# Kernel optimization log

Hardware: AMD Instinct MI355X
Metric: run time of the kernel (lower is better)

The kernel has to match this reference:

```python
import jax, jax.numpy as jnp
import numpy as np

N = 8192        # batch_size == num nodes == num hyperedges
D = 512         # hidden_dim
H_HEADS = 8
HD = D // H_HEADS
TOP_K = 16
EPS = 1e-5      # LayerNorm eps


def setup_inputs() -> dict:
    key = jax.random.key(0)
    ks = jax.random.split(key, 10)
    def rn(k, shape, scale=0.02):
        return jax.random.normal(k, shape, dtype=jnp.float32) * scale
    return {
        "x0": jax.random.normal(ks[0], (N, D), dtype=jnp.float32),
        "x1": jax.random.normal(ks[1], (N, D), dtype=jnp.float32),
        # modality projections: Linear -> ReLU -> LayerNorm (per modality)
        "w_p0": rn(ks[2], (D, D)), "b_p0": jnp.zeros((D,), jnp.float32),
        "g0": jnp.ones((D,), jnp.float32), "beta0": jnp.zeros((D,), jnp.float32),
        "w_p1": rn(ks[3], (D, D)), "b_p1": jnp.zeros((D,), jnp.float32),
        "g1": jnp.ones((D,), jnp.float32), "beta1": jnp.zeros((D,), jnp.float32),
        # MultiheadAttention packed in-proj + out-proj
        "in_w": rn(ks[4], (3 * D, D)), "in_b": jnp.zeros((3 * D,), jnp.float32),
        "out_w": rn(ks[5], (D, D)), "out_b": jnp.zeros((D,), jnp.float32),
        # edge weight predictor MLP
        "ew_w1": rn(ks[6], (D // 2, D)), "ew_b1": jnp.zeros((D // 2,), jnp.float32),
        "ew_w2": rn(ks[7], (1, D // 2)), "ew_b2": jnp.zeros((1,), jnp.float32),
    }


def _layernorm(x, g, b):
    m = x.mean(-1, keepdims=True)
    v = ((x - m) ** 2).mean(-1, keepdims=True)
    return (x - m) * jax.lax.rsqrt(v + EPS) * g + b


def _forward(x0, x1, w_p0, b_p0, g0, beta0, w_p1, b_p1, g1, beta1,
             in_w, in_b, out_w, out_b, ew_w1, ew_b1, ew_w2, ew_b2):
    # per-modality projection: Linear -> ReLU -> LayerNorm
    p0 = _layernorm(jax.nn.relu(x0 @ w_p0.T + b_p0), g0, beta0)
    p1 = _layernorm(jax.nn.relu(x1 @ w_p1.T + b_p1), g1, beta1)
    seq = jnp.stack([p0, p1], axis=1)                       # [N, 2, D]
    # cross-modal MHA (self-attention over the 2 modality tokens)
    qkv = seq @ in_w.T + in_b                               # [N, 2, 3D]
    q, k, v = jnp.split(qkv, 3, axis=-1)
    q = q.reshape(N, 2, H_HEADS, HD)
    k = k.reshape(N, 2, H_HEADS, HD)
    v = v.reshape(N, 2, H_HEADS, HD)
    scores = jnp.einsum('bqhd,bkhd->bhqk', q, k) / jnp.sqrt(jnp.float32(HD))
    attn = jax.nn.softmax(scores, axis=-1)                  # [N, h, 2, 2]
    ctx = jnp.einsum('bhqk,bkhd->bqhd', attn, v).reshape(N, 2, D)
    attended = ctx @ out_w.T + out_b                        # [N, 2, D]
    fused = attended.mean(axis=1)                           # [N, D]
    # node-node attention similarity, row-softmax
    sim = jax.nn.softmax(fused @ fused.T, axis=1)           # [N, N]
    _, idx = jax.lax.top_k(sim, TOP_K)                      # [N, K]
    vals = jnp.take_along_axis(sim, idx, axis=1)            # [N, K]
    rows = jnp.arange(N)
    # H[i,i]=1 first, then H[neighbor, i] = sim[i, neighbor] (may overwrite diag)
    H = jnp.zeros((N, N), sim.dtype).at[rows, rows].set(1.0)
    H = H.at[idx, rows[:, None]].set(vals)
    colsum = H.sum(axis=0)
    H = H.at[rows, rows].set(jnp.where(colsum == 0, 1.0, H[rows, rows]))
    # edge weights
    hidden = jax.nn.relu(fused @ ew_w1.T + ew_b1)
    ew = jax.nn.sigmoid(hidden @ ew_w2.T + ew_b2)[:, 0]     # [N]
    ew = jnp.maximum(ew, 1e-8)
    return H, ew


def reference(x0, x1, w_p0, b_p0, g0, beta0, w_p1, b_p1, g1, beta1,
              in_w, in_b, out_w, out_b, ew_w1, ew_b1, ew_w2, ew_b2):
    return _forward(x0, x1, w_p0, b_p0, g0, beta0, w_p1, b_p1, g1, beta1,
                    in_w, in_b, out_w, out_b, ew_w1, ew_b1, ew_w2, ew_b2)
```

## Files before the change

### kernel.cpp

```cpp
#include <hip/hip_runtime.h>
#include <hip/hip_bf16.h>

#define NN 8192
#define DD 512

typedef unsigned short u16;
typedef __bf16 bf16_t;
typedef bf16_t bf16x8 __attribute__((ext_vector_type(8)));
typedef float f32x4 __attribute__((ext_vector_type(4)));

__device__ __forceinline__ float bf2f(u16 h) {
    union { unsigned u; float f; } v; v.u = ((unsigned)h) << 16; return v.f;
}
__device__ __forceinline__ float bflo(unsigned u) {
    union { unsigned u; float f; } v; v.u = u << 16; return v.f;
}
__device__ __forceinline__ float bfhi(unsigned u) {
    union { unsigned u; float f; } v; v.u = u & 0xFFFF0000u; return v.f;
}
__device__ __forceinline__ u16 f2bf(float f) {
    union { float f; unsigned u; } v; v.f = f;
    unsigned r = v.u + 0x7fffu + ((v.u >> 16) & 1u);
    return (u16)(r >> 16);
}

__global__ __launch_bounds__(256) void cvt7(
        const float* __restrict__ s0, u16* __restrict__ d0,
        const float* __restrict__ s1, u16* __restrict__ d1,
        const float* __restrict__ s2, u16* __restrict__ d2,
        const float* __restrict__ s3, u16* __restrict__ d3,
        const float* __restrict__ s4, u16* __restrict__ d4,
        const float* __restrict__ s5, u16* __restrict__ d5,
        const float* __restrict__ s6, u16* __restrict__ d6) {
    size_t v = ((size_t)blockIdx.x * 256 + threadIdx.x) * 8;
    const float* s; u16* d; size_t off;
    if (v < 4194304)      { s = s0; d = d0; off = v; }
    else if (v < 8388608) { s = s1; d = d1; off = v - 4194304; }
    else if (v < 8650752) { s = s2; d = d2; off = v - 8388608; }
    else if (v < 8912896) { s = s3; d = d3; off = v - 8650752; }
    else if (v < 9699328) { s = s4; d = d4; off = v - 8912896; }
    else if (v < 9961472) { s = s5; d = d5; off = v - 9699328; }
    else                  { s = s6; d = d6; off = v - 9961472; }
    float4 a = *(const float4*)(s + off);
    float4 b = *(const float4*)(s + off + 4);
    ushort4 o0 = make_ushort4(f2bf(a.x), f2bf(a.y), f2bf(a.z), f2bf(a.w));
    ushort4 o1 = make_ushort4(f2bf(b.x), f2bf(b.y), f2bf(b.z), f2bf(b.w));
    *(ushort4*)(d + off) = o0;
    *(ushort4*)(d + off + 4) = o1;
}

#define EPS_LDS 136
template<bool RELU, bool BIAS, bool SPLIT>
__global__ __launch_bounds__(256) void gemm_bt(const u16* __restrict__ A,
        const u16* __restrict__ B, const float* __restrict__ bias,
        const u16* __restrict__ B2, const float* __restrict__ bias2, int halfY,
        u16* __restrict__ C, int M, int Nc, int K) {
    __shared__ alignas(16) u16 Smem[128 * EPS_LDS];
    u16* As = Smem;
    u16* Bs = Smem + 128 * 64;
    const int t = threadIdx.x;
    const int lane = t & 63;
    const int wave = t >> 6;
    const int wm = (wave >> 1) * 64;
    const int wn = (wave & 1) * 64;
    const int rowA = blockIdx.y * 128;
    const int rowB = blockIdx.x * 128;
    if (SPLIT && (int)blockIdx.y >= halfY) { B = B2; bias = bias2; }

    f32x4 acc[4][4] = {};
    const int mrow = lane & 15;
    const int kk = (lane >> 4) * 8;

    for (int k0 = 0; k0 < K; k0 += 64) {
        __syncthreads();
        #pragma unroll
        for (int r = 0; r < 4; ++r) {
            int chunk = r * 256 + t;
            const u16* srcA = A + (size_t)(rowA + (chunk >> 3)) * K + k0 + (chunk & 7) * 8;
            __builtin_amdgcn_global_load_lds(
                (const __attribute__((address_space(1))) void*)srcA,
                (__attribute__((address_space(3))) void*)(As + chunk * 8), 16, 0, 0);
            const u16* srcB = B + (size_t)(rowB + (chunk >> 3)) * K + k0 + (chunk & 7) * 8;
            __builtin_amdgcn_global_load_lds(
                (const __attribute__((address_space(1))) void*)srcB,
                (__attribute__((address_space(3))) void*)(Bs + chunk * 8), 16, 0, 0);
        }
        __syncthreads();
        #pragma unroll
        for (int ks = 0; ks < 64; ks += 32) {
            bf16x8 af[4], bfv[4];
            #pragma unroll
            for (int i = 0; i < 4; ++i)
                af[i] = *(const bf16x8*)(As + (wm + i * 16 + mrow) * 64 + ks + kk);
            #pragma unroll
            for (int j = 0; j < 4; ++j)
                bfv[j] = *(const bf16x8*)(Bs + (wn + j * 16 + mrow) * 64 + ks + kk);
            #pragma unroll
            for (int i = 0; i < 4; ++i)
                #pragma unroll
                for (int j = 0; j < 4; ++j)
                    acc[i][j] = __builtin_amdgcn_mfma_f32_16x16x32_bf16(af[i], bfv[j], acc[i][j], 0, 0, 0);
        }
    }

    __syncthreads();
    const int er0 = wm + (lane >> 4) * 4;
    const int ec0 = wn + (lane & 15);
    #pragma unroll
    for (int j = 0; j < 4; ++j) {
        int c = ec0 + j * 16;
        float bv = BIAS ? bias[rowB + c] : 0.0f;
        #pragma unroll
        for (int i = 0; i < 4; ++i) {
            #pragma unroll
            for (int r = 0; r < 4; ++r) {
                float v = acc[i][j][r] + bv;
                if (RELU) v = fmaxf(v, 0.0f);
                Smem[(er0 + i * 16 + r) * EPS_LDS + c] = f2bf(v);
            }
        }
    }
    __syncthreads();
    #pragma unroll
    for (int pass = 0; pass < 8; ++pass) {
        int chunk = pass * 256 + t;
        int rloc = chunk >> 4, coff = (chunk & 15) * 8;
        bf16x8 v = *(const bf16x8*)(Smem + rloc * EPS_LDS + coff);
        *(bf16x8*)(C + (size_t)(rowA + rloc) * Nc + rowB + coff) = v;
    }
}

#define SYM_LDS 129
__global__ __launch_bounds__(256) void gemm_sym(const u16* __restrict__ F,
        u16* __restrict__ C) {
    __shared__ alignas(16) u16 Smem[128 * SYM_LDS];
    const int bx = blockIdx.x, by = blockIdx.y;
    if (bx < by) return;
    u16* As = Smem;
    u16* Bs = Smem + 128 * 64;
    const int t = threadIdx.x;
    const int lane = t & 63;
    const int wave = t >> 6;
    const int wm = (wave >> 1) * 64;
    const int wn = (wave & 1) * 64;
    const int rowI = by * 128;
    const int rowJ = bx * 128;

    f32x4 acc[4][4] = {};
    const int mrow = lane & 15;
    const int kk = (lane >> 4) * 8;

    for (int k0 = 0; k0 < DD; k0 += 64) {
        __syncthreads();
        #pragma unroll
        for (int r = 0; r < 4; ++r) {
            int chunk = r * 256 + t;
            const u16* srcA = F + (size_t)(rowI + (chunk >> 3)) * DD + k0 + (chunk & 7) * 8;
            __builtin_amdgcn_global_load_lds(
                (const __attribute__((address_space(1))) void*)srcA,
                (__attribute__((address_space(3))) void*)(As + chunk * 8), 16, 0, 0);
            const u16* srcB = F + (size_t)(rowJ + (chunk >> 3)) * DD + k0 + (chunk & 7) * 8;
            __builtin_amdgcn_global_load_lds(
                (const __attribute__((address_space(1))) void*)srcB,
                (__attribute__((address_space(3))) void*)(Bs + chunk * 8), 16, 0, 0);
        }
        __syncthreads();
        #pragma unroll
        for (int ks = 0; ks < 64; ks += 32) {
            bf16x8 af[4], bfv[4];
            #pragma unroll
            for (int i = 0; i < 4; ++i)
                af[i] = *(const bf16x8*)(As + (wm + i * 16 + mrow) * 64 + ks + kk);
            #pragma unroll
            for (int j = 0; j < 4; ++j)
                bfv[j] = *(const bf16x8*)(Bs + (wn + j * 16 + mrow) * 64 + ks + kk);
            #pragma unroll
            for (int i = 0; i < 4; ++i)
                #pragma unroll
                for (int j = 0; j < 4; ++j)
                    acc[i][j] = __builtin_amdgcn_mfma_f32_16x16x32_bf16(af[i], bfv[j], acc[i][j], 0, 0, 0);
        }
    }

    __syncthreads();
    const int er0 = wm + (lane >> 4) * 4;
    const int ec0 = wn + (lane & 15);
    #pragma unroll
    for (int j = 0; j < 4; ++j) {
        int c = ec0 + j * 16;
        #pragma unroll
        for (int i = 0; i < 4; ++i) {
            #pragma unroll
            for (int r = 0; r < 4; ++r)
                Smem[(er0 + i * 16 + r) * SYM_LDS + c] = f2bf(acc[i][j][r]);
        }
    }
    __syncthreads();
    #pragma unroll
    for (int pass = 0; pass < 8; ++pass) {
        int chunk = pass * 256 + t;
        int rloc = chunk >> 4, coff = (chunk & 15) * 8;
        union { u16 us[8]; bf16x8 v; } buf;
        #pragma unroll
        for (int k = 0; k < 8; ++k) buf.us[k] = Smem[rloc * SYM_LDS + coff + k];
        *(bf16x8*)(C + (size_t)(rowI + rloc) * NN + rowJ + coff) = buf.v;
    }
    if (bx != by) {
        #pragma unroll
        for (int pass = 0; pass < 8; ++pass) {
            int chunk = pass * 256 + t;
            int tr = chunk >> 4, roff = (chunk & 15) * 8;
            union { u16 us[8]; bf16x8 v; } buf;
            #pragma unroll
            for (int k = 0; k < 8; ++k) buf.us[k] = Smem[(roff + k) * SYM_LDS + tr];
            *(bf16x8*)(C + (size_t)(rowJ + tr) * NN + rowI + roff) = buf.v;
        }
    }
}

__global__ __launch_bounds__(256) void ln2_kernel(const u16* __restrict__ y,
        const float* __restrict__ g0, const float* __restrict__ b0,
        const float* __restrict__ g1, const float* __restrict__ b1,
        u16* __restrict__ seq) {
    __shared__ float sred[4];
    int n = blockIdx.x, t = threadIdx.x;
    int modality = n >> 13, node = n & (NN - 1);
    const float* g = modality ? g1 : g0;
    const float* b = modality ? b1 : b0;
    const u16* yr = y + (size_t)n * DD;
    float x0 = bf2f(yr[t]), x1 = bf2f(yr[t + 256]);
    float s = x0 + x1;
    for (int off = 32; off; off >>= 1) s += __shfl_xor(s, off);
    if ((t & 63) == 0) sred[t >> 6] = s;
    __syncthreads();
    float mean = (sred[0] + sred[1] + sred[2] + sred[3]) * (1.0f / DD);
    __syncthreads();
    float d0 = x0 - mean, d1 = x1 - mean;
    float vs = d0 * d0 + d1 * d1;
    for (int off = 32; off; off >>= 1) vs += __shfl_xor(vs, off);
    if ((t & 63) == 0) sred[t >> 6] = vs;
    __syncthreads();
    float var = (sred[0] + sred[1] + sred[2] + sred[3]) * (1.0f / DD);
    float inv = rsqrtf(var + 1e-5f);
    u16* out = seq + (size_t)node * (2 * DD) + modality * DD;
    out[t]       = f2bf(d0 * inv * g[t]       + b[t]);
    out[t + 256] = f2bf(d1 * inv * g[t + 256] + b[t + 256]);
}

__global__ __launch_bounds__(256) void attn_kernel(const u16* __restrict__ qkv,
        u16* __restrict__ ctxm) {
    int gid = blockIdx.x * 4 + (threadIdx.x >> 6);
    int lane = threadIdx.x & 63;
    int n = gid >> 3, h = gid & 7;
    const u16* r0 = qkv + (size_t)(n * 2) * 1536;
    const u16* r1 = r0 + 1536;
    float q0 = bf2f(r0[h * 64 + lane]);
    float k0 = bf2f(r0[512 + h * 64 + lane]);
    float v0 = bf2f(r0[1024 + h * 64 + lane]);
    float q1 = bf2f(r1[h * 64 + lane]);
    float k1 = bf2f(r1[512 + h * 64 + lane]);
    float v1 = bf2f(r1[1024 + h * 64 + lane]);
    float p00 = q0 * k0, p01 = q0 * k1, p10 = q1 * k0, p11 = q1 * k1;
    for (int off = 32; off; off >>= 1) {
        p00 += __shfl_xor(p00, off);
        p01 += __shfl_xor(p01, off);
        p10 += __shfl_xor(p10, off);
        p11 += __shfl_xor(p11, off);
    }
    const float sc = 0.125f;
    float s00 = p00 * sc, s01 = p01 * sc, s10 = p10 * sc, s11 = p11 * sc;
    float m0 = fmaxf(s00, s01), e00 = __expf(s00 - m0), e01 = __expf(s01 - m0);
    float a00 = e00 / (e00 + e01), a01 = e01 / (e00 + e01);
    float m1 = fmaxf(s10, s11), e10 = __expf(s10 - m1), e11 = __expf(s11 - m1);
    float a10 = e10 / (e10 + e11), a11 = e11 / (e10 + e11);
    float c0 = a00 * v0 + a01 * v1;
    float c1 = a10 * v0 + a11 * v1;
    ctxm[(size_t)n * 512 + h * 64 + lane] = f2bf(0.5f * (c0 + c1));
}

__global__ __launch_bounds__(256) void topk_bf16(const u16* __restrict__ S,
        float* __restrict__ topv, int* __restrict__ topi) {
    const float NEG = -3e38f;
    int row = blockIdx.x * 4 + (threadIdx.x >> 6);
    int lane = threadIdx.x & 63;
    const u16* Sr = S + (size_t)row * NN;

    float m = NEG, l = 0.0f;
    float t1v = NEG, t2v = NEG;
    int t1i = 0x7FFFFFFF, t2i = 0x7FFFFFFF;

    #pragma unroll
    for (int p = 0; p < 16; ++p) {
        uint4 raw = *(const uint4*)(Sr + p * 512 + lane * 8);
        int base = p * 512 + lane * 8;
        #pragma unroll
        for (int q = 0; q < 4; ++q) {
            unsigned w = (&raw.x)[q];
            #pragma unroll
            for (int h = 0; h < 2; ++h) {
                float x = h ? bfhi(w) : bflo(w);
                int xi = base + q * 2 + h;
                if (x > m) { l = l * __expf(m - x) + 1.0f; m = x; }
                else l += __expf(x - m);
                bool g1 = x > t1v, g2 = x > t2v;
                t2v = g1 ? t1v : (g2 ? x : t2v);
                t2i = g1 ? t1i : (g2 ? xi : t2i);
                t1v = g1 ? x : t1v;
                t1i = g1 ? xi : t1i;
            }
        }
    }
    #pragma unroll
    for (int off = 32; off; off >>= 1) {
        float om = __shfl_xor(m, off);
        float ol = __shfl_xor(l, off);
        float nm = fmaxf(m, om);
        l = l * __expf(m - nm) + ol * __expf(om - nm);
        m = nm;
    }

    unsigned mk0 = 0, mk1 = 0, mk2 = 0, mk3 = 0;
    float cv = t1v; int ci = t1i;
    float bv = t2v; int bi = t2i;
    for (int r = 0; r < 16; ++r) {
        float wv = cv; int wi = ci;
        #pragma unroll
        for (int off = 32; off; off >>= 1) {
            float ov = __shfl_xor(wv, off);
            int oi = __shfl_xor(wi, off);
            if (ov > wv || (ov == wv && oi < wi)) { wv = ov; wi = oi; }
        }
        if (lane == 0) {
            topv[(size_t)row * 16 + r] = __expf(wv - m) / l;
            topi[(size_t)row * 16 + r] = wi;
        }
        if (wi == ci) {
            int slot = ((wi >> 9) << 3) | (wi & 7);
            unsigned bit = 1u << (slot & 31);
            if (slot < 32) mk0 |= bit; else if (slot < 64) mk1 |= bit;
            else if (slot < 96) mk2 |= bit; else mk3 |= bit;
            cv = bv; ci = bi;
            bv = NEG; bi = 0x7FFFFFFF;
            if (ci == 0x7FFFFFFF) {
                float nb = NEG; int ni = 0x7FFFFFFF;
                #pragma unroll
                for (int p = 0; p < 16; ++p) {
                    uint4 raw = *(const uint4*)(Sr + p * 512 + lane * 8);
                    int base = p * 512 + lane * 8;
                    #pragma unroll
                    for (int q = 0; q < 4; ++q) {
                        unsigned w = (&raw.x)[q];
                        #pragma unroll
                        for (int h = 0; h < 2; ++h) {
                            int sl = p * 8 + q * 2 + h;
                            unsigned mw = (sl < 32) ? mk0 : (sl < 64) ? mk1
                                        : (sl < 96) ? mk2 : mk3;
                            float x = ((mw >> (sl & 31)) & 1u) ? NEG
                                    : (h ? bfhi(w) : bflo(w));
                            if (x > nb) { nb = x; ni = base + q * 2 + h; }
                        }
                    }
                }
                cv = nb; ci = ni;
            }
        }
    }
}

__global__ __launch_bounds__(256) void scatter_diag(const float* __restrict__ topv,
        const int* __restrict__ topi, float* __restrict__ H) {
    int tk = blockIdx.x * 256 + threadIdx.x;
    if (tk < NN * 16) {
        int i = tk >> 4;
        int idx = topi[tk];
        H[(size_t)idx * NN + i] = topv[tk];
    } else {
        int c = tk - NN * 16;
        const int* ti = topi + c * 16;
        bool self = false;
        #pragma unroll
        for (int j = 0; j < 16; ++j) self |= (ti[j] == c);
        if (!self) H[(size_t)c * NN + c] = 1.0f;
    }
}

__global__ __launch_bounds__(256) void ew_kernel(const u16* __restrict__ hidden,
        const float* __restrict__ w2, const float* __restrict__ b2, float* __restrict__ out) {
    int n = blockIdx.x * 4 + (threadIdx.x >> 6);
    int lane = threadIdx.x & 63;
    const u16* hr = hidden + (size_t)n * 256;
    float s = 0.0f;
    #pragma unroll
    for (int p = 0; p < 4; ++p) s += bf2f(hr[lane + p * 64]) * w2[lane + p * 64];
    for (int off = 32; off; off >>= 1) s += __shfl_xor(s, off);
    if (lane == 0) {
        float z = s + b2[0];
        float sig = 1.0f / (1.0f + __expf(-z));
        out[n] = fmaxf(sig, 1e-8f);
    }
}

extern "C" void kernel_launch(void* const* d_in, const int* in_sizes, int n_in,
                              void* d_out, int out_size, void* d_ws, size_t ws_size,
                              hipStream_t stream) {
    const float* x0    = (const float*)d_in[0];
    const float* x1    = (const float*)d_in[1];
    const float* w_p0  = (const float*)d_in[2];
    const float* b_p0  = (const float*)d_in[3];
    const float* g0    = (const float*)d_in[4];
    const float* beta0 = (const float*)d_in[5];
    const float* w_p1  = (const float*)d_in[6];
    const float* b_p1  = (const float*)d_in[7];
    const float* g1    = (const float*)d_in[8];
    const float* beta1 = (const float*)d_in[9];
    const float* in_w  = (const float*)d_in[10];
    const float* in_b  = (const float*)d_in[11];
    const float* out_w = (const float*)d_in[12];
    const float* out_b = (const float*)d_in[13];
    const float* ew_w1 = (const float*)d_in[14];
    const float* ew_b1 = (const float*)d_in[15];
    const float* ew_w2 = (const float*)d_in[16];
    const float* ew_b2 = (const float*)d_in[17];

    float* Hf = (float*)d_out;
    float* ew_out = Hf + (size_t)NN * NN;

    u16* Hu = (u16*)d_out;
    u16* x0b    = Hu;
    u16* x1b    = Hu + 4194304;
    u16* y01    = Hu + 8388608;
    u16* seq    = Hu + 16777216;
    u16* qkv    = Hu + 25165824;
    u16* ctxm   = Hu + 50331648;
    u16* hidden = Hu + 54525952;
    u16* wp0b   = Hu + 60817408;
    u16* wp1b   = wp0b + 262144;
    u16* inwb   = wp1b + 262144;
    u16* outwb  = inwb + 786432;
    u16* eww1b  = outwb + 262144;
    u16* Sb     = Hu + 67108864;
    char* ws = (char*)d_ws;
    u16* fusedB = (u16*)ws;
    float* topv = (float*)(ws + (8u << 20));
    int*   topi = (int*)(ws + (8u << 20) + 524288);

    dim3 blk(256);
    const int BIG = 1 << 30;
    cvt7<<<dim3(4928), blk, 0, stream>>>(x0, x0b, x1, x1b, w_p0, wp0b, w_p1, wp1b,
                                         in_w, inwb, out_w, outwb, ew_w1, eww1b);
    gemm_bt<true, true, true><<<dim3(4, 128), blk, 0, stream>>>(
        x0b, wp0b, b_p0, wp1b, b_p1, 64, y01, 2 * NN, DD, DD);
    ln2_kernel<<<dim3(2 * NN), blk, 0, stream>>>(y01, g0, beta0, g1, beta1, seq);
    gemm_bt<false, true, false><<<dim3(12, 128), blk, 0, stream>>>(
        seq, inwb, in_b, nullptr, nullptr, BIG, qkv, 2 * NN, 1536, DD);
    attn_kernel<<<dim3(NN * 8 / 4), blk, 0, stream>>>(qkv, ctxm);
    gemm_bt<false, true, false><<<dim3(4, 64), blk, 0, stream>>>(
        ctxm, outwb, out_b, nullptr, nullptr, BIG, fusedB, NN, DD, DD);
    gemm_bt<true, true, false><<<dim3(2, 64), blk, 0, stream>>>(
        fusedB, eww1b, ew_b1, nullptr, nullptr, BIG, hidden, NN, 256, DD);
    ew_kernel<<<dim3(NN / 4), blk, 0, stream>>>(hidden, ew_w2, ew_b2, ew_out);
    gemm_sym<<<dim3(64, 64), blk, 0, stream>>>(fusedB, Sb);
    topk_bf16<<<dim3(NN / 4), blk, 0, stream>>>(Sb, topv, topi);
    hipMemsetAsync(Hf, 0, (size_t)NN * NN * sizeof(float), stream);
    scatter_diag<<<dim3((NN * 16 + NN) / 256), blk, 0, stream>>>(topv, topi, Hf);
}
```

Baseline: 690.9 us.

## Fuse QK score computation into QKV GEMM epilogue and slim attention kernel

The QKV projection GEMM now pairs each head's Q and K columns in one tile and computes the 2x2 per-head attention scores in its epilogue. It writes only the scores and the V projection instead of the full QKV tensor. The attention kernel then reads the small score array plus V, and averages the attention weights before mixing the V rows. This removes the round-trip of Q and K through global memory and the shuffle reductions, at the cost of a more specialised GEMM kernel and scores computed from bf16-rounded Q and K.

```diff
diff --git a/kernel.cpp b/kernel.cpp
--- a/kernel.cpp
+++ b/kernel.cpp
@@ -130,6 +130,101 @@
     }
 }
 
+__global__ __launch_bounds__(256) void gemm_qkv(const u16* __restrict__ A,
+        const u16* __restrict__ B, const float* __restrict__ bias,
+        u16* __restrict__ V, float* __restrict__ scores) {
+    __shared__ alignas(16) u16 Smem[128 * EPS_LDS];
+    u16* As = Smem;
+    u16* Bs = Smem + 128 * 64;
+    const int t = threadIdx.x;
+    const int lane = t & 63;
+    const int wave = t >> 6;
+    const int wm = (wave >> 1) * 64;
+    const int wn = (wave & 1) * 64;
+    const int c = blockIdx.x;
+    const int rowA = blockIdx.y * 128;
+    const bool isQK = (c < 8);
+
+    f32x4 acc[4][4] = {};
+    const int mrow = lane & 15;
+    const int kk = (lane >> 4) * 8;
+
+    for (int k0 = 0; k0 < DD; k0 += 64) {
+        __syncthreads();
+        #pragma unroll
+        for (int r = 0; r < 4; ++r) {
+            int chunk = r * 256 + t;
+            int rr = chunk >> 3;
+            int brow = isQK ? (c * 64 + rr + ((rr >= 64) ? 448 : 0))
+                            : (1024 + (c - 8) * 128 + rr);
+            const u16* srcA = A + (size_t)(rowA + rr) * DD + k0 + (chunk & 7) * 8;
+            __builtin_amdgcn_global_load_lds(
+                (const __attribute__((address_space(1))) void*)srcA,
+                (__attribute__((address_space(3))) void*)(As + chunk * 8), 16, 0, 0);
+            const u16* srcB = B + (size_t)brow * DD + k0 + (chunk & 7) * 8;
+            __builtin_amdgcn_global_load_lds(
+                (const __attribute__((address_space(1))) void*)srcB,
+                (__attribute__((address_space(3))) void*)(Bs + chunk * 8), 16, 0, 0);
+        }
+        __syncthreads();
+        #pragma unroll
+        for (int ks = 0; ks < 64; ks += 32) {
+            bf16x8 af[4], bfv[4];
+            #pragma unroll
+            for (int i = 0; i < 4; ++i)
+                af[i] = *(const bf16x8*)(As + (wm + i * 16 + mrow) * 64 + ks + kk);
+            #pragma unroll
+            for (int j = 0; j < 4; ++j)
+                bfv[j] = *(const bf16x8*)(Bs + (wn + j * 16 + mrow) * 64 + ks + kk);
+            #pragma unroll
+            for (int i = 0; i < 4; ++i)
+                #pragma unroll
+                for (int j = 0; j < 4; ++j)
+                    acc[i][j] = __builtin_amdgcn_mfma_f32_16x16x32_bf16(af[i], bfv[j], acc[i][j], 0, 0, 0);
+        }
+    }
+
+    __syncthreads();
+    const int er0 = wm + (lane >> 4) * 4;
+    const int ec0 = wn + (lane & 15);
+    #pragma unroll
+    for (int j = 0; j < 4; ++j) {
+        int cc = ec0 + j * 16;
+        int bcol = isQK ? ((cc < 64) ? c * 64 + cc : 448 + c * 64 + cc)
+                        : (1024 + (c - 8) * 128 + cc);
+        float bv = bias[bcol];
+        #pragma unroll
+        for (int i = 0; i < 4; ++i) {
+            #pragma unroll
+            for (int r = 0; r < 4; ++r)
+                Smem[(er0 + i * 16 + r) * EPS_LDS + cc] = f2bf(acc[i][j][r] + bv);
+        }
+    }
+    __syncthreads();
+    if (isQK) {
+        int nd = t >> 2, cb = t & 3, tt = cb >> 1, ss = cb & 1;
+        const u16* qrow = Smem + (2 * nd + tt) * EPS_LDS;
+        const u16* krow = Smem + (2 * nd + ss) * EPS_LDS + 64;
+        float s = 0.0f;
+        #pragma unroll
+        for (int d8 = 0; d8 < 8; ++d8) {
+            bf16x8 qv = *(const bf16x8*)(qrow + d8 * 8);
+            bf16x8 kv = *(const bf16x8*)(krow + d8 * 8);
+            #pragma unroll
+            for (int u = 0; u < 8; ++u) s += (float)qv[u] * (float)kv[u];
+        }
+        scores[(size_t)(rowA / 2 + nd) * 32 + c * 4 + cb] = s * 0.125f;
+    } else {
+        #pragma unroll
+        for (int pass = 0; pass < 8; ++pass) {
+            int chunk = pass * 256 + t;
+            int rloc = chunk >> 4, coff = (chunk & 15) * 8;
+            bf16x8 v = *(const bf16x8*)(Smem + rloc * EPS_LDS + coff);
+            *(bf16x8*)(V + (size_t)(rowA + rloc) * 512 + (c - 8) * 128 + coff) = v;
+        }
+    }
+}
+
 #define SYM_LDS 129
 __global__ __launch_bounds__(256) void gemm_sym(const u16* __restrict__ F,
         u16* __restrict__ C) {
@@ -247,35 +342,25 @@
     out[t + 256] = f2bf(d1 * inv * g[t + 256] + b[t + 256]);
 }
 
-__global__ __launch_bounds__(256) void attn_kernel(const u16* __restrict__ qkv,
-        u16* __restrict__ ctxm) {
-    int gid = blockIdx.x * 4 + (threadIdx.x >> 6);
+__global__ __launch_bounds__(256) void attn_v(const float* __restrict__ scores,
+        const u16* __restrict__ V, u16* __restrict__ ctxm) {
+    int n = blockIdx.x * 4 + (threadIdx.x >> 6);
     int lane = threadIdx.x & 63;
-    int n = gid >> 3, h = gid & 7;
-    const u16* r0 = qkv + (size_t)(n * 2) * 1536;
-    const u16* r1 = r0 + 1536;
-    float q0 = bf2f(r0[h * 64 + lane]);
-    float k0 = bf2f(r0[512 + h * 64 + lane]);
-    float v0 = bf2f(r0[1024 + h * 64 + lane]);
-    float q1 = bf2f(r1[h * 64 + lane]);
-    float k1 = bf2f(r1[512 + h * 64 + lane]);
-    float v1 = bf2f(r1[1024 + h * 64 + lane]);
-    float p00 = q0 * k0, p01 = q0 * k1, p10 = q1 * k0, p11 = q1 * k1;
-    for (int off = 32; off; off >>= 1) {
-        p00 += __shfl_xor(p00, off);
-        p01 += __shfl_xor(p01, off);
-        p10 += __shfl_xor(p10, off);
-        p11 += __shfl_xor(p11, off);
-    }
-    const float sc = 0.125f;
-    float s00 = p00 * sc, s01 = p01 * sc, s10 = p10 * sc, s11 = p11 * sc;
+    int h = lane >> 3;
+    float4 sc = *(const float4*)(scores + (size_t)n * 32 + h * 4);
+    float s00 = sc.x, s01 = sc.y, s10 = sc.z, s11 = sc.w;
     float m0 = fmaxf(s00, s01), e00 = __expf(s00 - m0), e01 = __expf(s01 - m0);
     float a00 = e00 / (e00 + e01), a01 = e01 / (e00 + e01);
     float m1 = fmaxf(s10, s11), e10 = __expf(s10 - m1), e11 = __expf(s11 - m1);
     float a10 = e10 / (e10 + e11), a11 = e11 / (e10 + e11);
-    float c0 = a00 * v0 + a01 * v1;
-    float c1 = a10 * v0 + a11 * v1;
-    ctxm[(size_t)n * 512 + h * 64 + lane] = f2bf(0.5f * (c0 + c1));
+    float al0 = 0.5f * (a00 + a10), al1 = 0.5f * (a01 + a11);
+    bf16x8 v0 = *(const bf16x8*)(V + (size_t)(2 * n) * 512 + lane * 8);
+    bf16x8 v1 = *(const bf16x8*)(V + (size_t)(2 * n + 1) * 512 + lane * 8);
+    union { u16 us[8]; bf16x8 v; } o;
+    #pragma unroll
+    for (int u = 0; u < 8; ++u)
+        o.us[u] = f2bf(al0 * (float)v0[u] + al1 * (float)v1[u]);
+    *(bf16x8*)(ctxm + (size_t)n * 512 + lane * 8) = o.v;
 }
 
 __global__ __launch_bounds__(256) void topk_bf16(const u16* __restrict__ S,
@@ -430,9 +515,10 @@
     u16* x1b    = Hu + 4194304;
     u16* y01    = Hu + 8388608;
     u16* seq    = Hu + 16777216;
-    u16* qkv    = Hu + 25165824;
+    u16* Vbuf   = Hu + 25165824;
     u16* ctxm   = Hu + 50331648;
     u16* hidden = Hu + 54525952;
+    float* scB  = (float*)(Hu + 58720256);
     u16* wp0b   = Hu + 60817408;
     u16* wp1b   = wp0b + 262144;
     u16* inwb   = wp1b + 262144;
@@ -451,9 +537,8 @@
     gemm_bt<true, true, true><<<dim3(4, 128), blk, 0, stream>>>(
         x0b, wp0b, b_p0, wp1b, b_p1, 64, y01, 2 * NN, DD, DD);
     ln2_kernel<<<dim3(2 * NN), blk, 0, stream>>>(y01, g0, beta0, g1, beta1, seq);
-    gemm_bt<false, true, false><<<dim3(12, 128), blk, 0, stream>>>(
-        seq, inwb, in_b, nullptr, nullptr, BIG, qkv, 2 * NN, 1536, DD);
-    attn_kernel<<<dim3(NN * 8 / 4), blk, 0, stream>>>(qkv, ctxm);
+    gemm_qkv<<<dim3(12, 128), blk, 0, stream>>>(seq, inwb, in_b, Vbuf, scB);
+    attn_v<<<dim3(NN / 4), blk, 0, stream>>>(scB, Vbuf, ctxm);
     gemm_bt<false, true, false><<<dim3(4, 64), blk, 0, stream>>>(
         ctxm, outwb, out_b, nullptr, nullptr, BIG, fusedB, NN, DD, DD);
     gemm_bt<true, true, false><<<dim3(2, 64), blk, 0, stream>>>(
```

New measurement: 687.9 us. Within noise of the previous version (-0.4%).
